# Kernel optimization log

Measured on AMD Instinct MI355X. Metric: run time of the kernel, lower is better.

## Reference

```python
import jax, jax.numpy as jnp
import numpy as np

B, H, W, C = 64, 28, 28, 384
WS, SHIFT, NH = 7, 3, 12
HD = C // NH
HID = 4 * C
N = WS * WS
NW = (H // WS) * (W // WS)
SCALE = HD ** -0.5
EPS = 1e-5


def _rel_pos_index():
    coords = np.stack(np.meshgrid(np.arange(WS), np.arange(WS), indexing='ij')).reshape(2, -1)
    rel = (coords[:, :, None] - coords[:, None, :]).transpose(1, 2, 0)
    rel[:, :, 0] += WS - 1
    rel[:, :, 1] += WS - 1
    rel[:, :, 0] *= 2 * WS - 1
    return rel.sum(-1)  # (N, N) int


def _attn_mask():
    img = np.zeros((H, W))
    cnt = 0
    sl = (slice(0, -WS), slice(-WS, -SHIFT), slice(-SHIFT, None))
    for hs in sl:
        for ws_ in sl:
            img[hs, ws_] = cnt
            cnt += 1
    mw = img.reshape(H // WS, WS, W // WS, WS).transpose(0, 2, 1, 3).reshape(NW, N)
    am = mw[:, None, :] - mw[:, :, None]
    return np.where(am != 0, -100.0, 0.0).astype(np.float32)  # (NW, N, N)


REL_IDX = jnp.asarray(_rel_pos_index())
MASK = jnp.asarray(_attn_mask())


def _ln(x, g, b):
    mu = jnp.mean(x, axis=-1, keepdims=True)
    var = jnp.mean(jnp.square(x - mu), axis=-1, keepdims=True)
    return (x - mu) * jax.lax.rsqrt(var + EPS) * g + b


def setup_inputs() -> dict:
    key = jax.random.key(0)
    ks = jax.random.split(key, 16)
    s = 0.02
    return {
        'x': jax.random.normal(ks[0], (B, H * W, C), jnp.float32),
        'qkv_w': jax.random.normal(ks[1], (C, 3 * C), jnp.float32) * s,
        'qkv_b': jnp.zeros((3 * C,), jnp.float32),
        'proj_w': jax.random.normal(ks[2], (C, C), jnp.float32) * s,
        'proj_b': jnp.zeros((C,), jnp.float32),
        'rpb_table': jax.random.normal(ks[3], ((2 * WS - 1) ** 2, NH), jnp.float32) * s,
        'norm1_g': jnp.ones((C,), jnp.float32),
        'norm1_b': jnp.zeros((C,), jnp.float32),
        'norm2_g': jnp.ones((C,), jnp.float32),
        'norm2_b': jnp.zeros((C,), jnp.float32),
        'fc1_w': jax.random.normal(ks[4], (C, HID), jnp.float32) * s,
        'fc1_b': jnp.zeros((HID,), jnp.float32),
        'fc2_w': jax.random.normal(ks[5], (HID, C), jnp.float32) * s,
        'fc2_b': jnp.zeros((C,), jnp.float32),
    }


def reference(x, qkv_w, qkv_b, proj_w, proj_b, rpb_table,
              norm1_g, norm1_b, norm2_g, norm2_b,
              fc1_w, fc1_b, fc2_w, fc2_b):
    shortcut = x
    h = _ln(x, norm1_g, norm1_b).reshape(B, H, W, C)
    # cyclic shift
    h = jnp.roll(h, (-SHIFT, -SHIFT), axis=(1, 2))
    # window partition -> (B*NW, N, C)
    xw = h.reshape(B, H // WS, WS, W // WS, WS, C).transpose(0, 1, 3, 2, 4, 5).reshape(B * NW, N, C)
    # qkv
    qkv = (xw @ qkv_w + qkv_b).reshape(B * NW, N, 3, NH, HD).transpose(2, 0, 3, 1, 4)
    q, k, v = qkv[0], qkv[1], qkv[2]  # (B*NW, NH, N, HD)
    attn = jnp.einsum('whnd,whmd->whnm', q * SCALE, k)  # (B*NW, NH, N, N)
    # relative position bias gather
    bias = rpb_table[REL_IDX.reshape(-1)].reshape(N, N, NH).transpose(2, 0, 1)  # (NH, N, N)
    attn = attn + bias[None]
    # shift mask
    attn = attn.reshape(B, NW, NH, N, N) + MASK[None, :, None]
    attn = jax.nn.softmax(attn.reshape(B * NW, NH, N, N), axis=-1)
    o = jnp.einsum('whnm,whmd->whnd', attn, v).transpose(0, 2, 1, 3).reshape(B * NW, N, C)
    o = o @ proj_w + proj_b
    # window reverse -> (B, H, W, C)
    h = o.reshape(B, H // WS, W // WS, WS, WS, C).transpose(0, 1, 3, 2, 4, 5).reshape(B, H, W, C)
    h = jnp.roll(h, (SHIFT, SHIFT), axis=(1, 2)).reshape(B, H * W, C)
    x = shortcut + h
    # MLP
    h2 = _ln(x, norm2_g, norm2_b)
    h2 = jax.nn.gelu(h2 @ fc1_w + fc1_b, approximate=False)
    h2 = h2 @ fc2_w + fc2_b
    return x + h2
```

## Files before the change

kernel.cpp:

```cpp
#include <hip/hip_runtime.h>
#include <hip/hip_bf16.h>
#include <math.h>

typedef unsigned short u16;
typedef __bf16 bf16x8 __attribute__((ext_vector_type(8)));
typedef float f32x4 __attribute__((ext_vector_type(4)));

#define M_ROWS 50176
#define SCALE_ 0.17677669529663687f

__device__ __forceinline__ float bf2f(u16 x){
  union { unsigned u; float f; } c; c.u = ((unsigned)x) << 16; return c.f;
}
__device__ __forceinline__ u16 f2bf(float f){
  union { float f; unsigned u; } c; c.f = f;
  unsigned u = c.u;
  u += 0x7fffu + ((u >> 16) & 1u);
  return (u16)(u >> 16);
}
__device__ __forceinline__ float ldf(const void* p, size_t i, int isbf){
  return isbf ? bf2f(((const u16*)p)[i]) : ((const float*)p)[i];
}

struct Ptrs { const void* p[14]; int sz[14]; };
__global__ __launch_bounds__(64) void probe_dtypes(Ptrs ps, int* flags){
  int i = blockIdx.x;
  const unsigned* w = (const unsigned*)ps.p[i];
  int nw = ps.sz[i] >> 1;
  if (nw < 1) nw = 1;
  int stride = nw >> 6; if (!stride) stride = 1;
  int lane = threadIdx.x;
  long idx = (long)lane * stride; if (idx >= nw) idx = nw - 1;
  unsigned v = w[idx];
  unsigned L = v & 0xFFFFu;
  int lexp = (int)((L >> 7) & 0xFF);
  bool vb = (L != 0) && (lexp >= 100) && (lexp <= 141);
  bool vf = (!vb) && (v != 0);
  unsigned long long mb = __ballot(vb), mf = __ballot(vf);
  if (lane == 0) flags[i] = (__popcll(mb) >= __popcll(mf)) ? 1 : 0;
}

__global__ void cvt_all(const void* qkv_b, const void* proj_b, const void* fc1_b, const void* fc2_b,
                        const void* n1g, const void* n1b, const void* n2g, const void* n2b,
                        const void* rpb, const int* __restrict__ flags, float* dst){
  int i = blockIdx.x * 256 + threadIdx.x;
  if (i >= 7020) return;
  const void* src; int loc, fi;
  if      (i < 1152){ src = qkv_b; loc = i;        fi = 2; }
  else if (i < 1536){ src = proj_b; loc = i - 1152; fi = 4; }
  else if (i < 3072){ src = fc1_b; loc = i - 1536; fi = 11; }
  else if (i < 3456){ src = fc2_b; loc = i - 3072; fi = 13; }
  else if (i < 3840){ src = n1g;  loc = i - 3456; fi = 6; }
  else if (i < 4224){ src = n1b;  loc = i - 3840; fi = 7; }
  else if (i < 4608){ src = n2g;  loc = i - 4224; fi = 8; }
  else if (i < 4992){ src = n2b;  loc = i - 4608; fi = 9; }
  else              { src = rpb;  loc = i - 4992; fi = 5; }
  dst[i] = ldf(src, loc, flags[fi]);
}

__global__ void transpose_k(const void* __restrict__ in, u16* __restrict__ out, int K, int N,
                            const int* __restrict__ flags, int fi){
  int tid = blockIdx.x * 256 + threadIdx.x;
  if (tid < K * N){
    int n = tid / K, k = tid - n * K;
    out[tid] = f2bf(ldf(in, (size_t)k * N + n, flags[fi]));
  }
}

__global__ __launch_bounds__(128) void ln1_kernel(const void* __restrict__ x, const float* __restrict__ g,
                                                  const float* __restrict__ bt, u16* __restrict__ xw,
                                                  const int* __restrict__ flags, int row0, int win0){
  int row = row0 + blockIdx.x;
  int bf = flags[0];
  size_t base = (size_t)row * 384;
  int t = threadIdx.x;
  float v0 = ldf(x, base + t, bf), v1 = ldf(x, base + t + 128, bf), v2 = ldf(x, base + t + 256, bf);
  float s = v0+v1+v2;
  float q = v0*v0+v1*v1+v2*v2;
  #pragma unroll
  for (int off = 32; off; off >>= 1){ s += __shfl_down(s, off); q += __shfl_down(q, off); }
  __shared__ float red[2][2];
  if ((t & 63) == 0){ red[t>>6][0] = s; red[t>>6][1] = q; }
  __syncthreads();
  float S = red[0][0] + red[1][0], Q = red[0][1] + red[1][1];
  float mu = S * (1.f/384.f);
  float var = Q * (1.f/384.f) - mu*mu;
  float rs = rsqrtf(var + 1e-5f);
  int b = row / 784; int hw = row - b*784; int h = hw / 28; int w = hw - h*28;
  int hs = h - 3; if (hs < 0) hs += 28;
  int ws = w - 3; if (ws < 0) ws += 28;
  int win = b*16 + (hs/7)*4 + (ws/7);
  int n = (hs%7)*7 + (ws%7);
  u16* orow = xw + ((size_t)(win - win0)*49 + n) * 384;
  orow[t]     = f2bf((v0 - mu)*rs*g[t]     + bt[t]);
  orow[t+128] = f2bf((v1 - mu)*rs*g[t+128] + bt[t+128]);
  orow[t+256] = f2bf((v2 - mu)*rs*g[t+256] + bt[t+256]);
}

__global__ __launch_bounds__(128) void ln2_kernel(const float* __restrict__ x, const float* __restrict__ g,
                                                  const float* __restrict__ bt, u16* __restrict__ xn, int row0){
  int row = row0 + blockIdx.x;
  const float* xr = x + (size_t)row * 384;
  int t = threadIdx.x;
  float v0 = xr[t], v1 = xr[t+128], v2 = xr[t+256];
  float s = v0+v1+v2;
  float q = v0*v0+v1*v1+v2*v2;
  #pragma unroll
  for (int off = 32; off; off >>= 1){ s += __shfl_down(s, off); q += __shfl_down(q, off); }
  __shared__ float red[2][2];
  if ((t & 63) == 0){ red[t>>6][0] = s; red[t>>6][1] = q; }
  __syncthreads();
  float S = red[0][0] + red[1][0], Q = red[0][1] + red[1][1];
  float mu = S * (1.f/384.f);
  float var = Q * (1.f/384.f) - mu*mu;
  float rs = rsqrtf(var + 1e-5f);
  u16* orow = xn + (size_t)blockIdx.x * 384;
  orow[t]     = f2bf((v0 - mu)*rs*g[t]     + bt[t]);
  orow[t+128] = f2bf((v1 - mu)*rs*g[t+128] + bt[t+128]);
  orow[t+256] = f2bf((v2 - mu)*rs*g[t+256] + bt[t+256]);
}

template<class Epi>
__global__ __launch_bounds__(256) void gemm_bt(const u16* __restrict__ A, const u16* __restrict__ Bt,
                                               int K, Epi epi){
  __shared__ __align__(16) u16 lds_a[128*40];
  __shared__ __align__(16) u16 lds_b[128*40];
  const int tid = threadIdx.x;
  const int lane = tid & 63, wid = tid >> 6;
  const int wm = wid >> 1, wn = wid & 1;
  const int quad = lane >> 4, l16 = lane & 15;
  const int m0 = blockIdx.x * 128, n0 = blockIdx.y * 128;

  f32x4 acc[4][4];
  #pragma unroll
  for (int i = 0; i < 4; i++)
    #pragma unroll
    for (int j = 0; j < 4; j++){ f32x4 z = {0.f,0.f,0.f,0.f}; acc[i][j] = z; }

  for (int k0 = 0; k0 < K; k0 += 32){
    #pragma unroll
    for (int it = 0; it < 2; it++){
      int c = tid + it*256;
      int row = c >> 2, k8 = (c & 3) << 3;
      *(uint4*)&lds_a[row*40 + k8] = *(const uint4*)&A[(size_t)(m0+row)*K + k0 + k8];
      *(uint4*)&lds_b[row*40 + k8] = *(const uint4*)&Bt[(size_t)(n0+row)*K + k0 + k8];
    }
    __syncthreads();
    bf16x8 af[4], bfr[4];
    #pragma unroll
    for (int i = 0; i < 4; i++){
      af[i]  = *(const bf16x8*)&lds_a[(wm*64 + i*16 + l16)*40 + quad*8];
      bfr[i] = *(const bf16x8*)&lds_b[(wn*64 + i*16 + l16)*40 + quad*8];
    }
    #pragma unroll
    for (int i = 0; i < 4; i++)
      #pragma unroll
      for (int j = 0; j < 4; j++)
        acc[i][j] = __builtin_amdgcn_mfma_f32_16x16x32_bf16(af[i], bfr[j], acc[i][j], 0, 0, 0);
    __syncthreads();
  }
  #pragma unroll
  for (int i = 0; i < 4; i++)
    #pragma unroll
    for (int j = 0; j < 4; j++)
      #pragma unroll
      for (int r = 0; r < 4; r++){
        int row = m0 + wm*64 + i*16 + quad*4 + r;
        int col = n0 + wn*64 + j*16 + l16;
        epi(acc[i][j][r], row, col);
      }
}

struct EpiQKV {
  const float* bias; u16 *q, *k, *v;
  __device__ __forceinline__ void operator()(float acc, int row, int col) const {
    float val = acc + bias[col];
    int which = col / 384; int cc = col - which*384;
    int head = cc >> 5, hd = cc & 31;
    int win = row / 49; int n = row - win*49;
    if (which == 0) val *= SCALE_;
    u16* dst = (which == 0) ? q : (which == 1) ? k : v;
    dst[((size_t)(win*12 + head)*49 + n)*32 + hd] = f2bf(val);
  }
};

struct EpiProj {
  const float* bias; const void* x; float* x1; const int* flags; int win0;
  __device__ __forceinline__ void operator()(float acc, int row, int col) const {
    int win = win0 + row / 49; int n = row - (row/49)*49;
    int b = win >> 4; int w16 = win & 15;
    int wh = w16 >> 2, ww = w16 & 3;
    int r = n / 7, cn = n - r*7;
    int h = wh*7 + r + 3; if (h >= 28) h -= 28;
    int w = ww*7 + cn + 3; if (w >= 28) w -= 28;
    size_t idx = ((size_t)b*784 + h*28 + w)*384 + col;
    x1[idx] = acc + bias[col] + ldf(x, idx, flags[0]);
  }
};

struct EpiFC1 {
  const float* bias; u16* hid;
  __device__ __forceinline__ void operator()(float acc, int row, int col) const {
    float x = acc + bias[col];
    float g = 0.5f * x * (1.0f + erff(x * 0.70710678118654752f));
    hid[(size_t)row*1536 + col] = f2bf(g);
  }
};

struct EpiFC2 {
  const float* bias; const float* x1; float* out; size_t row_off;
  __device__ __forceinline__ void operator()(float acc, int row, int col) const {
    size_t idx = (row_off + (size_t)row)*384 + col;
    out[idx] = x1[idx] + acc + bias[col];
  }
};

__global__ __launch_bounds__(256) void attn_kernel(const u16* __restrict__ q, const u16* __restrict__ kk,
                                                   const u16* __restrict__ v, const float* __restrict__ rpbf,
                                                   u16* __restrict__ o){
  __shared__ __align__(16) u16 qs[64*32];
  __shared__ __align__(16) u16 ks[64*32];
  __shared__ __align__(16) u16 vt[32*72];
  __shared__ __align__(16) u16 ps[64*72];
  __shared__ float ss[64*68];
  __shared__ float rpbs[169];

  int blk = blockIdx.x;
  int win = blk / 12, head = blk - win*12;
  int tid = threadIdx.x, lane = tid & 63, wid = tid >> 6;
  int quad = lane >> 4, l16 = lane & 15;
  size_t base = (size_t)blk * 1568;

  for (int e = tid; e < 64*32; e += 256){
    qs[e] = (e < 1568) ? q[base + e]  : (u16)0;
    ks[e] = (e < 1568) ? kk[base + e] : (u16)0;
  }
  for (int e = tid; e < 32*64; e += 256){
    int d = e >> 6, j = e & 63;
    vt[d*72 + j] = (j < 49) ? v[base + j*32 + d] : (u16)0;
  }
  for (int e = tid; e < 64*72; e += 256) ps[e] = 0;
  if (tid < 169) rpbs[tid] = rpbf[tid*12 + head];
  __syncthreads();

  int i0 = wid * 16;
  bf16x8 aq = *(const bf16x8*)&qs[(i0 + l16)*32 + quad*8];
  int w16 = win & 15; int wh = w16 >> 2; int ww = w16 & 3;
  f32x4 zero = {0.f,0.f,0.f,0.f};
  #pragma unroll
  for (int nt = 0; nt < 4; nt++){
    bf16x8 bk = *(const bf16x8*)&ks[(nt*16 + l16)*32 + quad*8];
    f32x4 c = __builtin_amdgcn_mfma_f32_16x16x32_bf16(aq, bk, zero, 0, 0, 0);
    #pragma unroll
    for (int r = 0; r < 4; r++){
      int i = i0 + quad*4 + r;
      int j = nt*16 + l16;
      float val = -1e9f;
      if (i < 49 && j < 49){
        int ir = i / 7, ic = i - ir*7, jr = j / 7, jc = j - jr*7;
        int idx = (ir - jr + 6)*13 + (ic - jc + 6);
        val = c[r] + rpbs[idx];
        int gih = wh*7 + ir, giw = ww*7 + ic;
        int gjh = wh*7 + jr, gjw = ww*7 + jc;
        int li = (gih < 21 ? 0 : (gih < 25 ? 1 : 2))*3 + (giw < 21 ? 0 : (giw < 25 ? 1 : 2));
        int lj = (gjh < 21 ? 0 : (gjh < 25 ? 1 : 2))*3 + (gjw < 21 ? 0 : (gjw < 25 ? 1 : 2));
        if (li != lj) val -= 100.f;
      }
      ss[i*68 + j] = val;
    }
  }
  __syncthreads();

  for (int r = wid; r < 49; r += 4){
    float x = ss[r*68 + lane];
    float mx = x;
    #pragma unroll
    for (int off = 32; off; off >>= 1) mx = fmaxf(mx, __shfl_xor(mx, off));
    float e = expf(x - mx);
    float sum = e;
    #pragma unroll
    for (int off = 32; off; off >>= 1) sum += __shfl_xor(sum, off);
    ps[r*72 + lane] = f2bf(e / sum);
  }
  __syncthreads();

  f32x4 accO[2] = {{0.f,0.f,0.f,0.f},{0.f,0.f,0.f,0.f}};
  #pragma unroll
  for (int s = 0; s < 2; s++){
    bf16x8 ap = *(const bf16x8*)&ps[(i0 + l16)*72 + s*32 + quad*8];
    #pragma unroll
    for (int nt = 0; nt < 2; nt++){
      bf16x8 bv = *(const bf16x8*)&vt[(nt*16 + l16)*72 + s*32 + quad*8];
      accO[nt] = __builtin_amdgcn_mfma_f32_16x16x32_bf16(ap, bv, accO[nt], 0, 0, 0);
    }
  }
  #pragma unroll
  for (int nt = 0; nt < 2; nt++)
    #pragma unroll
    for (int r = 0; r < 4; r++){
      int i = i0 + quad*4 + r;
      if (i < 49){
        int col = nt*16 + l16;
        o[((size_t)win*49 + i)*384 + head*32 + col] = f2bf(accO[nt][r]);
      }
    }
}

extern "C" void kernel_launch(void* const* d_in, const int* in_sizes, int n_in,
                              void* d_out, int out_size, void* d_ws, size_t ws_size,
                              hipStream_t stream){
  (void)n_in; (void)out_size;
  const void* x      = d_in[0];
  const void* qkv_w  = d_in[1];
  const void* qkv_b  = d_in[2];
  const void* proj_w = d_in[3];
  const void* proj_b = d_in[4];
  const void* rpb    = d_in[5];
  const void* n1g    = d_in[6];
  const void* n1b    = d_in[7];
  const void* n2g    = d_in[8];
  const void* n2b    = d_in[9];
  const void* fc1_w  = d_in[10];
  const void* fc1_b  = d_in[11];
  const void* fc2_w  = d_in[12];
  const void* fc2_b  = d_in[13];
  float* out = (float*)d_out;

  char* ws = (char*)d_ws;
  size_t off = 0;
  auto alloc = [&](size_t bytes)->void*{
    void* p = ws + off; off = (off + bytes + 255) & ~(size_t)255; return p;
  };
  int*   flags  = (int*)  alloc(14*4);
  float* prm    = (float*)alloc(7020*4);
  u16*   qkv_wt = (u16*)  alloc((size_t)384*1152*2);
  u16*   proj_wt= (u16*)  alloc((size_t)384*384*2);
  u16*   fc1_wt = (u16*)  alloc((size_t)384*1536*2);
  u16*   fc2_wt = (u16*)  alloc((size_t)1536*384*2);
  size_t fixed_end = off;
  size_t avail = (ws_size > fixed_end) ? ws_size - fixed_end : 0;

  int attn_wins = 128;
  if      ((size_t)1024*150528 <= avail) attn_wins = 1024;
  else if ((size_t)512 *150528 <= avail) attn_wins = 512;
  else if ((size_t)256 *150528 <= avail) attn_wins = 256;

  int mlp_rows = 1792;
  if      ((size_t)50176*3840 <= avail) mlp_rows = 50176;
  else if ((size_t)25088*3840 <= avail) mlp_rows = 25088;
  else if ((size_t)12544*3840 <= avail) mlp_rows = 12544;
  else if ((size_t)6272 *3840 <= avail) mlp_rows = 6272;

  u16* scr = (u16*)(ws + fixed_end);
  u16* xw  = scr;
  u16* qs  = scr + (size_t)attn_wins*49*384;
  u16* ksp = qs  + (size_t)attn_wins*12*49*32;
  u16* vs  = ksp + (size_t)attn_wins*12*49*32;
  u16* xn  = scr;
  u16* hid = scr + (size_t)mlp_rows*384;

  float* p_qkv_b = prm;
  float* p_proj_b= prm + 1152;
  float* p_fc1_b = prm + 1536;
  float* p_fc2_b = prm + 3072;
  float* p_n1g   = prm + 3456;
  float* p_n1b   = prm + 3840;
  float* p_n2g   = prm + 4224;
  float* p_n2b   = prm + 4608;
  float* p_rpb   = prm + 4992;

  Ptrs ps;
  for (int i = 0; i < 14; i++){ ps.p[i] = d_in[i]; ps.sz[i] = in_sizes[i]; }
  probe_dtypes<<<14, 64, 0, stream>>>(ps, flags);

  cvt_all<<<28, 256, 0, stream>>>(qkv_b, proj_b, fc1_b, fc2_b, n1g, n1b, n2g, n2b, rpb, flags, prm);

  transpose_k<<<(384*1152+255)/256, 256, 0, stream>>>(qkv_w,  qkv_wt, 384, 1152, flags, 1);
  transpose_k<<<(384*384 +255)/256, 256, 0, stream>>>(proj_w, proj_wt, 384, 384, flags, 3);
  transpose_k<<<(384*1536+255)/256, 256, 0, stream>>>(fc1_w,  fc1_wt, 384, 1536, flags, 10);
  transpose_k<<<(1536*384+255)/256, 256, 0, stream>>>(fc2_w,  fc2_wt, 1536, 384, flags, 12);

  int nch = 1024 / attn_wins;
  for (int c = 0; c < nch; c++){
    int win0 = c * attn_wins, row0 = win0 * 49;
    int mrows = attn_wins * 49;
    ln1_kernel<<<mrows, 128, 0, stream>>>(x, p_n1g, p_n1b, xw, flags, row0, win0);
    gemm_bt<<<dim3(mrows/128, 9), 256, 0, stream>>>(xw, qkv_wt, 384, EpiQKV{p_qkv_b, qs, ksp, vs});
    attn_kernel<<<attn_wins*12, 256, 0, stream>>>(qs, ksp, vs, p_rpb, xw);
    gemm_bt<<<dim3(mrows/128, 3), 256, 0, stream>>>(xw, proj_wt, 384, EpiProj{p_proj_b, x, out, flags, win0});
  }

  for (int r0 = 0; r0 < M_ROWS; r0 += mlp_rows){
    ln2_kernel<<<mlp_rows, 128, 0, stream>>>(out, p_n2g, p_n2b, xn, r0);
    gemm_bt<<<dim3(mlp_rows/128, 12), 256, 0, stream>>>(xn, fc1_wt, 384, EpiFC1{p_fc1_b, hid});
    gemm_bt<<<dim3(mlp_rows/128, 3),  256, 0, stream>>>(hid, fc2_wt, 1536,
        EpiFC2{p_fc2_b, out, out, (size_t)r0});
  }
}
```

Before: 849.6 us.

## Precompute bias-mask tables, transpose V in QKV epilogue, register softmax in attention

```diff
diff --git a/kernel.cpp b/kernel.cpp
--- a/kernel.cpp
+++ b/kernel.cpp
@@ -64,6 +64,27 @@
   if (tid < K * N){
     int n = tid / K, k = tid - n * K;
     out[tid] = f2bf(ldf(in, (size_t)k * N + n, flags[fi]));
+  }
+}
+
+__global__ __launch_bounds__(256) void build_bm(const float* __restrict__ rpbf, u16* __restrict__ bm_g){
+  int wt = blockIdx.x / 12, head = blockIdx.x - wt*12;
+  u16* dst = bm_g + (size_t)blockIdx.x * 4096;
+  bool he = (wt & 2), we = (wt & 1);
+  for (int e = threadIdx.x; e < 4096; e += 256){
+    int i = e >> 6, j = e & 63;
+    float val;
+    if (i >= 49) val = 0.f;
+    else if (j >= 49) val = -1e9f;
+    else {
+      int ir = i/7, ic = i - ir*7, jr = j/7, jc = j - jr*7;
+      int idx = (ir - jr + 6)*13 + (ic - jc + 6);
+      val = rpbf[idx*12 + head];
+      int li = (he ? (ir < 4 ? 1 : 2) : 0)*3 + (we ? (ic < 4 ? 1 : 2) : 0);
+      int lj = (he ? (jr < 4 ? 1 : 2) : 0)*3 + (we ? (jc < 4 ? 1 : 2) : 0);
+      if (li != lj) val -= 100.f;
+    }
+    dst[e] = f2bf(val);
   }
 }
 
@@ -172,15 +193,19 @@
 }
 
 struct EpiQKV {
-  const float* bias; u16 *q, *k, *v;
+  const float* bias; u16 *q, *k, *vt;
   __device__ __forceinline__ void operator()(float acc, int row, int col) const {
     float val = acc + bias[col];
     int which = col / 384; int cc = col - which*384;
     int head = cc >> 5, hd = cc & 31;
     int win = row / 49; int n = row - win*49;
-    if (which == 0) val *= SCALE_;
-    u16* dst = (which == 0) ? q : (which == 1) ? k : v;
-    dst[((size_t)(win*12 + head)*49 + n)*32 + hd] = f2bf(val);
+    if (which == 0){
+      q[((size_t)(win*12 + head)*49 + n)*32 + hd] = f2bf(val * SCALE_);
+    } else if (which == 1){
+      k[((size_t)(win*12 + head)*49 + n)*32 + hd] = f2bf(val);
+    } else {
+      vt[((size_t)(win*12 + head)*32 + hd)*64 + n] = f2bf(val);
+    }
   }
 };
 
@@ -216,93 +241,76 @@
 };
 
 __global__ __launch_bounds__(256) void attn_kernel(const u16* __restrict__ q, const u16* __restrict__ kk,
-                                                   const u16* __restrict__ v, const float* __restrict__ rpbf,
+                                                   const u16* __restrict__ vt_g, const u16* __restrict__ bm_g,
                                                    u16* __restrict__ o){
-  __shared__ __align__(16) u16 qs[64*32];
-  __shared__ __align__(16) u16 ks[64*32];
-  __shared__ __align__(16) u16 vt[32*72];
   __shared__ __align__(16) u16 ps[64*72];
-  __shared__ float ss[64*68];
-  __shared__ float rpbs[169];
-
+  __shared__ __align__(16) u16 bms[64*72];
   int blk = blockIdx.x;
   int win = blk / 12, head = blk - win*12;
   int tid = threadIdx.x, lane = tid & 63, wid = tid >> 6;
   int quad = lane >> 4, l16 = lane & 15;
   size_t base = (size_t)blk * 1568;
 
-  for (int e = tid; e < 64*32; e += 256){
-    qs[e] = (e < 1568) ? q[base + e]  : (u16)0;
-    ks[e] = (e < 1568) ? kk[base + e] : (u16)0;
-  }
-  for (int e = tid; e < 32*64; e += 256){
-    int d = e >> 6, j = e & 63;
-    vt[d*72 + j] = (j < 49) ? v[base + j*32 + d] : (u16)0;
-  }
-  for (int e = tid; e < 64*72; e += 256) ps[e] = 0;
-  if (tid < 169) rpbs[tid] = rpbf[tid*12 + head];
+  int w16 = win & 15;
+  int wt = (((w16 >> 2) == 3) ? 2 : 0) + (((w16 & 3) == 3) ? 1 : 0);
+  const u16* bsrc = bm_g + (size_t)(wt*12 + head) * 4096;
+  #pragma unroll
+  for (int it = 0; it < 2; it++){
+    int e = tid + it*256;
+    int row = e >> 3, c8 = (e & 7) << 3;
+    *(uint4*)&bms[row*72 + c8] = *(const uint4*)&bsrc[row*64 + c8];
+  }
+
+  int i0 = wid * 16;
+  bf16x8 aq = *(const bf16x8*)&q[base + (size_t)(i0 + l16)*32 + quad*8];
+  f32x4 zero = {0.f,0.f,0.f,0.f};
+  f32x4 c[4];
+  #pragma unroll
+  for (int nt = 0; nt < 4; nt++){
+    bf16x8 bk = *(const bf16x8*)&kk[base + (size_t)(nt*16 + l16)*32 + quad*8];
+    c[nt] = __builtin_amdgcn_mfma_f32_16x16x32_bf16(aq, bk, zero, 0, 0, 0);
+  }
   __syncthreads();
 
-  int i0 = wid * 16;
-  bf16x8 aq = *(const bf16x8*)&qs[(i0 + l16)*32 + quad*8];
-  int w16 = win & 15; int wh = w16 >> 2; int ww = w16 & 3;
-  f32x4 zero = {0.f,0.f,0.f,0.f};
-  #pragma unroll
-  for (int nt = 0; nt < 4; nt++){
-    bf16x8 bk = *(const bf16x8*)&ks[(nt*16 + l16)*32 + quad*8];
-    f32x4 c = __builtin_amdgcn_mfma_f32_16x16x32_bf16(aq, bk, zero, 0, 0, 0);
+  #pragma unroll
+  for (int r = 0; r < 4; r++){
+    int i = i0 + quad*4 + r;
+    float v0 = c[0][r] + bf2f(bms[i*72 +      l16]);
+    float v1 = c[1][r] + bf2f(bms[i*72 + 16 + l16]);
+    float v2 = c[2][r] + bf2f(bms[i*72 + 32 + l16]);
+    float v3 = c[3][r] + bf2f(bms[i*72 + 48 + l16]);
+    float m = fmaxf(fmaxf(v0, v1), fmaxf(v2, v3));
+    #pragma unroll
+    for (int off = 1; off < 16; off <<= 1) m = fmaxf(m, __shfl_xor(m, off));
+    float e0 = __expf(v0 - m), e1 = __expf(v1 - m), e2 = __expf(v2 - m), e3 = __expf(v3 - m);
+    float s = e0 + e1 + e2 + e3;
+    #pragma unroll
+    for (int off = 1; off < 16; off <<= 1) s += __shfl_xor(s, off);
+    float inv = 1.f / s;
+    ps[i*72 +      l16] = f2bf(e0 * inv);
+    ps[i*72 + 16 + l16] = f2bf(e1 * inv);
+    ps[i*72 + 32 + l16] = f2bf(e2 * inv);
+    ps[i*72 + 48 + l16] = f2bf(e3 * inv);
+  }
+
+  size_t vbase = (size_t)blk * 2048;
+  f32x4 accO[2] = {{0.f,0.f,0.f,0.f},{0.f,0.f,0.f,0.f}};
+  #pragma unroll
+  for (int s2 = 0; s2 < 2; s2++){
+    bf16x8 ap = *(const bf16x8*)&ps[(i0 + l16)*72 + s2*32 + quad*8];
+    #pragma unroll
+    for (int nt = 0; nt < 2; nt++){
+      bf16x8 bv = *(const bf16x8*)&vt_g[vbase + (size_t)(nt*16 + l16)*64 + s2*32 + quad*8];
+      accO[nt] = __builtin_amdgcn_mfma_f32_16x16x32_bf16(ap, bv, accO[nt], 0, 0, 0);
+    }
+  }
+  #pragma unroll
+  for (int nt = 0; nt < 2; nt++)
     #pragma unroll
     for (int r = 0; r < 4; r++){
       int i = i0 + quad*4 + r;
-      int j = nt*16 + l16;
-      float val = -1e9f;
-      if (i < 49 && j < 49){
-        int ir = i / 7, ic = i - ir*7, jr = j / 7, jc = j - jr*7;
-        int idx = (ir - jr + 6)*13 + (ic - jc + 6);
-        val = c[r] + rpbs[idx];
-        int gih = wh*7 + ir, giw = ww*7 + ic;
-        int gjh = wh*7 + jr, gjw = ww*7 + jc;
-        int li = (gih < 21 ? 0 : (gih < 25 ? 1 : 2))*3 + (giw < 21 ? 0 : (giw < 25 ? 1 : 2));
-        int lj = (gjh < 21 ? 0 : (gjh < 25 ? 1 : 2))*3 + (gjw < 21 ? 0 : (gjw < 25 ? 1 : 2));
-        if (li != lj) val -= 100.f;
-      }
-      ss[i*68 + j] = val;
-    }
-  }
-  __syncthreads();
-
-  for (int r = wid; r < 49; r += 4){
-    float x = ss[r*68 + lane];
-    float mx = x;
-    #pragma unroll
-    for (int off = 32; off; off >>= 1) mx = fmaxf(mx, __shfl_xor(mx, off));
-    float e = expf(x - mx);
-    float sum = e;
-    #pragma unroll
-    for (int off = 32; off; off >>= 1) sum += __shfl_xor(sum, off);
-    ps[r*72 + lane] = f2bf(e / sum);
-  }
-  __syncthreads();
-
-  f32x4 accO[2] = {{0.f,0.f,0.f,0.f},{0.f,0.f,0.f,0.f}};
-  #pragma unroll
-  for (int s = 0; s < 2; s++){
-    bf16x8 ap = *(const bf16x8*)&ps[(i0 + l16)*72 + s*32 + quad*8];
-    #pragma unroll
-    for (int nt = 0; nt < 2; nt++){
-      bf16x8 bv = *(const bf16x8*)&vt[(nt*16 + l16)*72 + s*32 + quad*8];
-      accO[nt] = __builtin_amdgcn_mfma_f32_16x16x32_bf16(ap, bv, accO[nt], 0, 0, 0);
-    }
-  }
-  #pragma unroll
-  for (int nt = 0; nt < 2; nt++)
-    #pragma unroll
-    for (int r = 0; r < 4; r++){
-      int i = i0 + quad*4 + r;
-      if (i < 49){
-        int col = nt*16 + l16;
-        o[((size_t)win*49 + i)*384 + head*32 + col] = f2bf(accO[nt][r]);
-      }
+      if (i < 49)
+        o[((size_t)win*49 + i)*384 + head*32 + nt*16 + l16] = f2bf(accO[nt][r]);
     }
 }
 
@@ -333,6 +341,7 @@
   };
   int*   flags  = (int*)  alloc(14*4);
   float* prm    = (float*)alloc(7020*4);
+  u16*   bm_g   = (u16*)  alloc((size_t)48*4096*2);
   u16*   qkv_wt = (u16*)  alloc((size_t)384*1152*2);
   u16*   proj_wt= (u16*)  alloc((size_t)384*384*2);
   u16*   fc1_wt = (u16*)  alloc((size_t)384*1536*2);
@@ -341,9 +350,9 @@
   size_t avail = (ws_size > fixed_end) ? ws_size - fixed_end : 0;
 
   int attn_wins = 128;
-  if      ((size_t)1024*150528 <= avail) attn_wins = 1024;
-  else if ((size_t)512 *150528 <= avail) attn_wins = 512;
-  else if ((size_t)256 *150528 <= avail) attn_wins = 256;
+  if      ((size_t)1024*162048 <= avail) attn_wins = 1024;
+  else if ((size_t)512 *162048 <= avail) attn_wins = 512;
+  else if ((size_t)256 *162048 <= avail) attn_wins = 256;
 
   int mlp_rows = 1792;
   if      ((size_t)50176*3840 <= avail) mlp_rows = 50176;
@@ -355,7 +364,7 @@
   u16* xw  = scr;
   u16* qs  = scr + (size_t)attn_wins*49*384;
   u16* ksp = qs  + (size_t)attn_wins*12*49*32;
-  u16* vs  = ksp + (size_t)attn_wins*12*49*32;
+  u16* vts = ksp + (size_t)attn_wins*12*49*32;
   u16* xn  = scr;
   u16* hid = scr + (size_t)mlp_rows*384;
 
@@ -374,19 +383,22 @@
   probe_dtypes<<<14, 64, 0, stream>>>(ps, flags);
 
   cvt_all<<<28, 256, 0, stream>>>(qkv_b, proj_b, fc1_b, fc2_b, n1g, n1b, n2g, n2b, rpb, flags, prm);
+  build_bm<<<48, 256, 0, stream>>>(p_rpb, bm_g);
 
   transpose_k<<<(384*1152+255)/256, 256, 0, stream>>>(qkv_w,  qkv_wt, 384, 1152, flags, 1);
   transpose_k<<<(384*384 +255)/256, 256, 0, stream>>>(proj_w, proj_wt, 384, 384, flags, 3);
   transpose_k<<<(384*1536+255)/256, 256, 0, stream>>>(fc1_w,  fc1_wt, 384, 1536, flags, 10);
   transpose_k<<<(1536*384+255)/256, 256, 0, stream>>>(fc2_w,  fc2_wt, 1536, 384, flags, 12);
+
+  hipMemsetAsync(vts, 0, (size_t)attn_wins*12*32*64*2, stream);
 
   int nch = 1024 / attn_wins;
   for (int c = 0; c < nch; c++){
     int win0 = c * attn_wins, row0 = win0 * 49;
     int mrows = attn_wins * 49;
     ln1_kernel<<<mrows, 128, 0, stream>>>(x, p_n1g, p_n1b, xw, flags, row0, win0);
-    gemm_bt<<<dim3(mrows/128, 9), 256, 0, stream>>>(xw, qkv_wt, 384, EpiQKV{p_qkv_b, qs, ksp, vs});
-    attn_kernel<<<attn_wins*12, 256, 0, stream>>>(qs, ksp, vs, p_rpb, xw);
+    gemm_bt<<<dim3(mrows/128, 9), 256, 0, stream>>>(xw, qkv_wt, 384, EpiQKV{p_qkv_b, qs, ksp, vts});
+    attn_kernel<<<attn_wins*12, 256, 0, stream>>>(qs, ksp, vts, bm_g, xw);
     gemm_bt<<<dim3(mrows/128, 3), 256, 0, stream>>>(xw, proj_wt, 384, EpiProj{p_proj_b, x, out, flags, win0});
   }
 
```

Result: faster. 811.2 us (-4.5%).
